# Kernel tuning notes

Measured on AMD Instinct MI355X. Metric: run time of the kernel, lower is better.

## Reference

```python
import jax, jax.numpy as jnp
import numpy as np

B, T, C = 2, 2048, 1024
H, GAMMA = 16, 8
D = C // H
SCALE = 1.0 / np.sqrt(D).astype(np.float32)


def setup_inputs() -> dict:
    key = jax.random.key(0)
    ks = jax.random.split(key, 6)
    w = 0.02
    return {
        'x': jax.random.normal(ks[0], (B, T, C), dtype=jnp.float32),
        'Wq': jax.random.normal(ks[1], (C, 2 * C), dtype=jnp.float32) * w,
        'Wk': jax.random.normal(ks[2], (C, 2 * C), dtype=jnp.float32) * w,
        'Wv': jax.random.normal(ks[3], (C, C), dtype=jnp.float32) * w,
        'Wo': jax.random.normal(ks[4], (C, C), dtype=jnp.float32) * w,
        'theta_offset': jax.random.normal(ks[5], (H,), dtype=jnp.float32) * 0.1,
    }


def _heads(t):
    # (B, T, C) -> (B, H, T, D)
    return t.reshape(B, T, H, D).transpose(0, 2, 1, 3)


def reference(x, Wq, Wk, Wv, Wo, theta_offset):
    q_raw = x @ Wq                      # (B, T, 2C)
    k_raw = x @ Wk                      # (B, T, 2C)
    v = _heads(x @ Wv)                  # (B, H, T, D)

    q_amp, q_phase = jnp.split(q_raw, 2, axis=-1)
    k_amp, k_phase = jnp.split(k_raw, 2, axis=-1)
    q_amp = jax.nn.softplus(_heads(q_amp))
    q_phase = _heads(q_phase)
    k_amp = jax.nn.softplus(_heads(k_amp))
    k_phase = _heads(k_phase)

    q_real = q_amp * jnp.cos(q_phase)
    q_imag = q_amp * jnp.sin(q_phase)
    k_real = k_amp * jnp.cos(k_phase)
    k_imag = k_amp * jnp.sin(k_phase)

    scores = (jnp.einsum('bhtd,bhsd->bhts', q_real, k_real)
              + jnp.einsum('bhtd,bhsd->bhts', q_imag, k_imag)) * SCALE

    # theta gating (active since T > GAMMA)
    cycle_ids = jnp.arange(T, dtype=jnp.float32) / GAMMA
    cycle_dist = cycle_ids[None, :] - cycle_ids[:, None]        # (T, T)
    theta_gate = jnp.cos(theta_offset[:, None, None] * cycle_dist)  # (H, T, T)
    scores = scores * theta_gate[None]

    causal = jnp.tril(jnp.ones((T, T), dtype=bool))
    scores = jnp.where(causal[None, None], scores, -jnp.inf)
    attn = jax.nn.softmax(scores, axis=-1)

    out = jnp.einsum('bhts,bhsd->bhtd', attn, v)
    out = out.transpose(0, 2, 1, 3).reshape(B, T, C)
    return out @ Wo
```

## Files before the change

### kernel.cpp

```cpp
#include <hip/hip_runtime.h>
#include <hip/hip_bf16.h>
#include <math.h>

#define Bc 2
#define Tc 2048
#define Cc 1024
#define Hc 16
#define Dc 64

typedef __attribute__((ext_vector_type(8))) short short8;
typedef __attribute__((ext_vector_type(4))) float f32x4;

#define L2E 1.44269504088896f
#define SM_M 20.0f

__device__ __forceinline__ short f2bf(float x) {
    unsigned u = __float_as_uint(x);
    u += 0x7fff + ((u >> 16) & 1);
    return (short)(u >> 16);
}
__device__ __forceinline__ unsigned pack2bf_fast(float a, float b) {
    unsigned ua = __float_as_uint(a) + 0x8000u;
    unsigned ub = __float_as_uint(b) + 0x8000u;
    return __builtin_amdgcn_perm(ub, ua, 0x07060302);
}
__device__ __forceinline__ float softplus_fast(float a) {
    return fmaxf(a, 0.f) + __logf(1.f + __expf(-fabsf(a)));
}

template <int EPI>
__global__ __launch_bounds__(256) void gemm_bt_mfma(
    const short* __restrict__ A, const short* __restrict__ Bt,
    float* __restrict__ Cf, short* __restrict__ Cb, short* __restrict__ Cb2,
    int M, int N, int K)
{
    __shared__ __attribute__((aligned(16))) short As[128 * 32];
    __shared__ __attribute__((aligned(16))) short Bs[128 * 32];

    const int tid = threadIdx.x;
    const int wave = tid >> 6, lane = tid & 63;
    const int quad = lane >> 4, c = lane & 15;
    const int wm = wave >> 1, wn = wave & 1;
    const int m0 = blockIdx.y * 128, n0 = blockIdx.x * 128;

    const int srow = lane >> 2;
    const int scol = (lane & 3) * 8;
    const short* Ag = A  + (size_t)(m0 + wave * 32 + srow) * K + scol;
    const short* Bg = Bt + (size_t)(n0 + wave * 32 + srow) * K + scol;
    short* AsW = As + (wave * 32) * 32;
    short* BsW = Bs + (wave * 32) * 32;

    f32x4 acc[4][4];
#pragma unroll
    for (int i = 0; i < 4; ++i)
#pragma unroll
        for (int j = 0; j < 4; ++j)
            acc[i][j] = (f32x4){0.f, 0.f, 0.f, 0.f};

    for (int k0 = 0; k0 < K; k0 += 32) {
        __syncthreads();
#pragma unroll
        for (int i = 0; i < 2; ++i) {
            __builtin_amdgcn_global_load_lds(
                (const __attribute__((address_space(1))) void*)(Ag + k0 + (size_t)i * 16 * K),
                (__attribute__((address_space(3))) void*)(AsW + i * 16 * 32), 16, 0, 0);
            __builtin_amdgcn_global_load_lds(
                (const __attribute__((address_space(1))) void*)(Bg + k0 + (size_t)i * 16 * K),
                (__attribute__((address_space(3))) void*)(BsW + i * 16 * 32), 16, 0, 0);
        }
        __syncthreads();

        short8 af[4], bf[4];
#pragma unroll
        for (int mt = 0; mt < 4; ++mt)
            af[mt] = *(const short8*)&As[(wm * 64 + mt * 16 + c) * 32 + quad * 8];
#pragma unroll
        for (int nt = 0; nt < 4; ++nt)
            bf[nt] = *(const short8*)&Bs[(wn * 64 + nt * 16 + c) * 32 + quad * 8];
#pragma unroll
        for (int mt = 0; mt < 4; ++mt)
#pragma unroll
            for (int nt = 0; nt < 4; ++nt)
                acc[mt][nt] = __builtin_amdgcn_mfma_f32_16x16x32_bf16(
                    af[mt], bf[nt], acc[mt][nt], 0, 0, 0);
    }

    if (EPI == 2) {
        const int g = n0 >> 7;
        const int isK = g >> 4;
        const int h = g & 15;
        const float scl = isK ? 1.f : 0.125f;
        short* dst = isK ? Cb2 : Cb;
#pragma unroll
        for (int mt = 0; mt < 4; ++mt) {
#pragma unroll
            for (int reg = 0; reg < 4; ++reg) {
                int m = m0 + wm * 64 + mt * 16 + quad * 4 + reg;
                int bb = m >> 11, tt = m & (Tc - 1);
                size_t base = (((size_t)bb * Hc + h) * Tc + tt) * 128;
#pragma unroll
                for (int nt = 0; nt < 2; ++nt) {
                    float amp = acc[mt][nt][reg];
                    float ph  = acc[mt][nt + 2][reg];
                    int d = wn * 32 + nt * 16 + c;
                    float sp = softplus_fast(amp) * scl;
                    float sn, cs;
                    __sincosf(ph, &sn, &cs);
                    dst[base + d]      = f2bf(sp * cs);
                    dst[base + d + 64] = f2bf(sp * sn);
                }
            }
        }
    } else {
#pragma unroll
        for (int mt = 0; mt < 4; ++mt) {
#pragma unroll
            for (int reg = 0; reg < 4; ++reg) {
                size_t row = m0 + wm * 64 + mt * 16 + quad * 4 + reg;
#pragma unroll
                for (int nt = 0; nt < 4; ++nt) {
                    size_t col = n0 + wn * 64 + nt * 16 + c;
                    if (EPI == 1) Cb[row * N + col] = f2bf(acc[mt][nt][reg]);
                    else          Cf[row * N + col] = acc[mt][nt][reg];
                }
            }
        }
    }
}

__global__ __launch_bounds__(256) void gemm_v2t(
    const short* __restrict__ A, const short* __restrict__ Bt,
    short* __restrict__ v2t)
{
    __shared__ __attribute__((aligned(16))) short As[128 * 32];
    __shared__ __attribute__((aligned(16))) short Bs[128 * 32];
    __shared__ __attribute__((aligned(16))) short tile[128 * 136];

    const int K = Cc;
    const int tid = threadIdx.x;
    const int wave = tid >> 6, lane = tid & 63;
    const int quad = lane >> 4, c = lane & 15;
    const int wm = wave >> 1, wn = wave & 1;
    const int m0 = blockIdx.y * 128, n0 = blockIdx.x * 128;

    const int srow = lane >> 2;
    const int scol = (lane & 3) * 8;
    const short* Ag = A  + (size_t)(m0 + wave * 32 + srow) * K + scol;
    const short* Bg = Bt + (size_t)(n0 + wave * 32 + srow) * K + scol;
    short* AsW = As + (wave * 32) * 32;
    short* BsW = Bs + (wave * 32) * 32;

    f32x4 acc[4][4];
#pragma unroll
    for (int i = 0; i < 4; ++i)
#pragma unroll
        for (int j = 0; j < 4; ++j)
            acc[i][j] = (f32x4){0.f, 0.f, 0.f, 0.f};

    for (int k0 = 0; k0 < K; k0 += 32) {
        __syncthreads();
#pragma unroll
        for (int i = 0; i < 2; ++i) {
            __builtin_amdgcn_global_load_lds(
                (const __attribute__((address_space(1))) void*)(Ag + k0 + (size_t)i * 16 * K),
                (__attribute__((address_space(3))) void*)(AsW + i * 16 * 32), 16, 0, 0);
            __builtin_amdgcn_global_load_lds(
                (const __attribute__((address_space(1))) void*)(Bg + k0 + (size_t)i * 16 * K),
                (__attribute__((address_space(3))) void*)(BsW + i * 16 * 32), 16, 0, 0);
        }
        __syncthreads();

        short8 af[4], bf[4];
#pragma unroll
        for (int mt = 0; mt < 4; ++mt)
            af[mt] = *(const short8*)&As[(wm * 64 + mt * 16 + c) * 32 + quad * 8];
#pragma unroll
        for (int nt = 0; nt < 4; ++nt)
            bf[nt] = *(const short8*)&Bs[(wn * 64 + nt * 16 + c) * 32 + quad * 8];
#pragma unroll
        for (int mt = 0; mt < 4; ++mt)
#pragma unroll
            for (int nt = 0; nt < 4; ++nt)
                acc[mt][nt] = __builtin_amdgcn_mfma_f32_16x16x32_bf16(
                    af[mt], bf[nt], acc[mt][nt], 0, 0, 0);
    }

#pragma unroll
    for (int mt = 0; mt < 4; ++mt)
#pragma unroll
        for (int reg = 0; reg < 4; ++reg) {
            int tl = wm * 64 + mt * 16 + quad * 4 + reg;
#pragma unroll
            for (int nt = 0; nt < 4; ++nt)
                tile[(wn * 64 + nt * 16 + c) * 136 + tl] = f2bf(acc[mt][nt][reg]);
        }
    __syncthreads();

    const int b = m0 >> 11, tl0 = m0 & (Tc - 1);
#pragma unroll
    for (int i = 0; i < 8; ++i) {
        int n = i * 16 + (tid >> 4);
        int t8 = (tid & 15) * 8;
        int ng = n0 + n, h = ng >> 6, d = ng & 63;
        *(short8*)&v2t[(((size_t)b * Hc + h) * Dc + d) * Tc + tl0 + t8] =
            *(const short8*)&tile[n * 136 + t8];
    }
}

__global__ __launch_bounds__(256) void xconv(const float* __restrict__ x,
                                             short* __restrict__ xb)
{
    int idx = blockIdx.x * 256 + threadIdx.x;
    float4 v = *(const float4*)&x[(size_t)idx * 4];
    short4 o = {f2bf(v.x), f2bf(v.y), f2bf(v.z), f2bf(v.w)};
    *(short4*)&xb[(size_t)idx * 4] = o;
}

__global__ __launch_bounds__(256) void wtrans_qk(const float* __restrict__ Wq,
                                                 const float* __restrict__ Wk,
                                                 short* __restrict__ Bt)
{
    __shared__ short tile[64][80];
    const int n0 = blockIdx.x * 64, k0 = blockIdx.y * 64;
    const int half = blockIdx.z;
    const float* W = half ? Wk : Wq;
    const int tid = threadIdx.x;
#pragma unroll
    for (int i = 0; i < 4; ++i) {
        int e = i * 256 + tid;
        int k = e >> 4, n4 = (e & 15) * 4;
        float4 v = *(const float4*)&W[(size_t)(k0 + k) * 2048 + n0 + n4];
        tile[k][n4]     = f2bf(v.x);
        tile[k][n4 + 1] = f2bf(v.y);
        tile[k][n4 + 2] = f2bf(v.z);
        tile[k][n4 + 3] = f2bf(v.w);
    }
    __syncthreads();
#pragma unroll
    for (int i = 0; i < 16; ++i) {
        int e = i * 256 + tid;
        int n = e >> 6, k = e & 63;
        int ng = n0 + n;
        int sub = ng >> 10, hh = (ng >> 6) & 15, dd = ng & 63;
        int r = (half * 16 + hh) * 128 + (dd >> 5) * 64 + sub * 32 + (dd & 31);
        Bt[(size_t)r * Cc + k0 + k] = tile[k][n];
    }
}

__global__ __launch_bounds__(256) void wtrans2(const float* __restrict__ Wv,
                                               const float* __restrict__ Wo,
                                               short* __restrict__ WtBase)
{
    __shared__ short tile[64][80];
    const int n0 = blockIdx.x * 64, k0 = blockIdx.y * 64;
    const float* W = blockIdx.z ? Wo : Wv;
    short* Wt = WtBase + (size_t)blockIdx.z * Cc * Cc;
    const int tid = threadIdx.x;
#pragma unroll
    for (int i = 0; i < 4; ++i) {
        int e = i * 256 + tid;
        int k = e >> 4, n4 = (e & 15) * 4;
        float4 v = *(const float4*)&W[(size_t)(k0 + k) * Cc + n0 + n4];
        tile[k][n4]     = f2bf(v.x);
        tile[k][n4 + 1] = f2bf(v.y);
        tile[k][n4 + 2] = f2bf(v.z);
        tile[k][n4 + 3] = f2bf(v.w);
    }
    __syncthreads();
#pragma unroll
    for (int i = 0; i < 16; ++i) {
        int e = i * 256 + tid;
        int n = e >> 6, k = e & 63;
        Wt[(size_t)(n0 + n) * Cc + k0 + k] = tile[k][n];
    }
}

__global__ __launch_bounds__(512, 4) void moire_attn6(
    const short* __restrict__ q2, const short* __restrict__ k2,
    const short* __restrict__ v2t, const float* __restrict__ theta,
    short* __restrict__ att)
{
    __shared__ __attribute__((aligned(16))) short Ks[2][64 * 128];
    __shared__ __attribute__((aligned(16))) short Vt[2][64 * 64];
    __shared__ __attribute__((aligned(16))) short Ps[8][16 * 64];

    const int tid = threadIdx.x;
    const int wave = tid >> 6, lane = tid & 63;
    const int quad = lane >> 4, c = lane & 15;
    const int tx = wave >> 2, wq = wave & 3;
    const int p = blockIdx.x, h = blockIdx.y, b = blockIdx.z;
    const int qx = tx ? (31 - p) : p;
    const int q0 = qx * 64;
    const float th = theta[h];

    const short* k2b = k2 + (size_t)(b * Hc + h) * Tc * 128;
    const short* v2b = v2t + (size_t)(b * Hc + h) * Dc * Tc;

    short8 qf[4];
    const short* qp = q2 + ((size_t)(b * Hc + h) * Tc + q0 + wq * 16 + c) * 128;
#pragma unroll
    for (int i = 0; i < 4; ++i)
        qf[i] = *(const short8*)(qp + i * 32 + quad * 8);

    const int t_l = wq * 16 + c;
    float x0 = th * 0.125f * (float)(q0 + t_l);
    float cb = __cosf(x0), sb = -__sinf(x0);
    float cOff[4][4], sOff[4][4];
#pragma unroll
    for (int mt = 0; mt < 4; ++mt)
#pragma unroll
        for (int reg = 0; reg < 4; ++reg) {
            float a = th * 0.125f * (float)(mt * 16 + quad * 4 + reg);
            cOff[mt][reg] = __cosf(a) * L2E;
            sOff[mt][reg] = __sinf(a) * L2E;
        }
    const float cD = __cosf(8.f * th), sD = __sinf(8.f * th);

    f32x4 oacc[4];
    float lsum = 0.f;
#pragma unroll
    for (int nt = 0; nt < 4; ++nt)
        oacc[nt] = (f32x4){0.f, 0.f, 0.f, 0.f};

    auto stageK = [&](int jts) {
        short* KsB = &Ks[jts & 1][0];
        const int s0 = jts * 64;
#pragma unroll
        for (int i = 0; i < 2; ++i) {
            int ch = i * 512 + tid;
            int row = ch >> 4, j = ch & 15;
            const short* src = k2b + (size_t)(s0 + row) * 128 + ((j ^ (row & 15)) << 3);
            __builtin_amdgcn_global_load_lds(
                (const __attribute__((address_space(1))) void*)src,
                (__attribute__((address_space(3))) void*)(KsB + (i * 512 + wave * 64) * 8),
                16, 0, 0);
        }
    };
    auto stageV = [&](int jts) {
        short* VtB = &Vt[jts & 1][0];
        const int s0 = jts * 64;
        int row = tid >> 3, j = tid & 7;
        const short* src = v2b + (size_t)row * Tc + s0 + ((j ^ (row & 7)) << 3);
        __builtin_amdgcn_global_load_lds(
            (const __attribute__((address_space(1))) void*)src,
            (__attribute__((address_space(3))) void*)(VtB + (wave * 64) * 8),
            16, 0, 0);
    };

    auto do_pv = [&](int jprev) {
        const short* VtB = &Vt[jprev & 1][0];
        short8 pf[2];
#pragma unroll
        for (int kk = 0; kk < 2; ++kk)
            pf[kk] = *(const short8*)&Ps[wave][c * 64 +
                         (((kk * 4 + quad) ^ (c & 7)) << 3)];
#pragma unroll
        for (int nt = 0; nt < 4; ++nt)
#pragma unroll
            for (int kk = 0; kk < 2; ++kk) {
                short8 vf = *(const short8*)&VtB[(nt * 16 + c) * 64 +
                             (((kk * 4 + quad) ^ (c & 7)) << 3)];
                oacc[nt] = __builtin_amdgcn_mfma_f32_16x16x32_bf16(
                    pf[kk], vf, oacc[nt], 0, 0, 0);
            }
    };

    auto do_s = [&](int jt) {
        const short* KsB = &Ks[jt & 1][0];
        const bool diag = (jt == qx);

        f32x4 s_acc[4];
#pragma unroll
        for (int mt = 0; mt < 4; ++mt) {
            f32x4 a = {0.f, 0.f, 0.f, 0.f};
#pragma unroll
            for (int kk = 0; kk < 4; ++kk) {
                short8 kf = *(const short8*)&KsB[(mt * 16 + c) * 128 +
                                                 (((kk * 4 + quad) ^ c) << 3)];
                a = __builtin_amdgcn_mfma_f32_16x16x32_bf16(kf, qf[kk], a, 0, 0, 0);
            }
            s_acc[mt] = a;
        }

#pragma unroll
        for (int mt = 0; mt < 4; ++mt) {
            float pv[4];
#pragma unroll
            for (int reg = 0; reg < 4; ++reg) {
                float g2 = cb * cOff[mt][reg] - sb * sOff[mt][reg];
                float arg = fmaf(s_acc[mt][reg], g2, -SM_M * L2E);
                if (diag && (mt * 16 + quad * 4 + reg) > t_l) arg = -1e30f;
                pv[reg] = exp2f(arg);
            }
            lsum += (pv[0] + pv[1]) + (pv[2] + pv[3]);
            uint2 pk = {pack2bf_fast(pv[0], pv[1]), pack2bf_fast(pv[2], pv[3])};
            int slot = ((mt * 2 + (quad >> 1)) ^ (c & 7));
            *(uint2*)&Ps[wave][c * 64 + slot * 8 + (quad & 1) * 4] = pk;
        }

        float ncb = cb * cD - sb * sD;
        sb = sb * cD + cb * sD;
        cb = ncb;
    };

    stageK(0);
    const int jtEnd = 31 - p;
    for (int jt = 0; jt <= jtEnd; ++jt) {
        __syncthreads();
        if (jt < jtEnd) stageK(jt + 1);
        stageV(jt);

        const bool doS  = (jt <= qx);
        const bool doPV = (jt >= 1) & (jt <= qx + 1);
        if (doS & doPV) {
            do_pv(jt - 1);
            do_s(jt);
        } else if (doS) {
            do_s(jt);
        } else if (doPV) {
            do_pv(jt - 1);
        }
    }

    __syncthreads();
    if (qx == jtEnd) do_pv(jtEnd);

    float l = lsum;
    l += __shfl_xor(l, 16);
    l += __shfl_xor(l, 32);
    float il = 1.f / l;
    float ilr[4];
#pragma unroll
    for (int reg = 0; reg < 4; ++reg)
        ilr[reg] = __shfl(il, quad * 4 + reg);
#pragma unroll
    for (int reg = 0; reg < 4; ++reg) {
        int t_g = q0 + wq * 16 + quad * 4 + reg;
#pragma unroll
        for (int nt = 0; nt < 4; ++nt)
            att[(size_t)(b * Tc + t_g) * Cc + h * Dc + nt * 16 + c] =
                f2bf(oacc[nt][reg] * ilr[reg]);
    }
}

extern "C" void kernel_launch(void* const* d_in, const int* in_sizes, int n_in,
                              void* d_out, int out_size, void* d_ws, size_t ws_size,
                              hipStream_t stream)
{
    const float* x     = (const float*)d_in[0];
    const float* Wq    = (const float*)d_in[1];
    const float* Wk    = (const float*)d_in[2];
    const float* Wv    = (const float*)d_in[3];
    const float* Wo    = (const float*)d_in[4];
    const float* theta = (const float*)d_in[5];
    float* out = (float*)d_out;

    const int M = Bc * Tc;
    char* ws = (char*)d_ws;
    const size_t MB = 1 << 20;
    short* xb   = (short*)(ws);
    short* Bqk  = (short*)(ws + 8 * MB);
    short* Wvt  = (short*)(ws + 16 * MB);
    short* Wot  = (short*)(ws + 18 * MB);
    short* v2t  = (short*)(ws + 28 * MB);
    short* attb = (short*)(ws + 36 * MB);
    short* q2   = (short*)(ws + 44 * MB);
    short* k2   = (short*)d_out;

    xconv<<<(size_t)M * Cc / 1024, 256, 0, stream>>>(x, xb);
    wtrans_qk<<<dim3(2048 / 64, Cc / 64, 2), 256, 0, stream>>>(Wq, Wk, Bqk);
    wtrans2<<<dim3(Cc / 64, Cc / 64, 2), 256, 0, stream>>>(Wv, Wo, Wvt);

    gemm_bt_mfma<2><<<dim3(4096 / 128, M / 128), 256, 0, stream>>>(
        xb, Bqk, nullptr, q2, k2, M, 4096, Cc);
    gemm_v2t<<<dim3(Cc / 128, M / 128), 256, 0, stream>>>(xb, Wvt, v2t);

    moire_attn6<<<dim3(16, Hc, Bc), 512, 0, stream>>>(q2, k2, v2t, theta, attb);

    gemm_bt_mfma<0><<<dim3(Cc / 128, M / 128), 256, 0, stream>>>(
        attb, Wot, out, nullptr, nullptr, M, Cc, Cc);
}
```

Baseline: 262.2 us.

## Replace QK projection GEMM with 256x256 pipelined direct-to-LDS MFMA kernel

The fused Q/K projection GEMM with its softplus/sincos epilogue moves from a 128x128 tile, 256-thread kernel to a 256x256 tile, 512-thread kernel. The new kernel double-buffers K=64 slices in LDS using global_load_lds with an XOR swizzle, and interleaves loads with MFMA quadrants under explicit barriers, vmcnt waits and setprio. The weight transpose row permutation changes so that amplitude and phase columns land in the new tile layout. The goal is to hide global latency and raise operand reuse in the largest GEMM. The cost is heavy LDS use (128KB per block) and a fragile hand-scheduled barrier and waitcnt pipeline.

```diff
diff --git a/kernel.cpp b/kernel.cpp
--- a/kernel.cpp
+++ b/kernel.cpp
@@ -28,10 +28,164 @@
     return fmaxf(a, 0.f) + __logf(1.f + __expf(-fabsf(a)));
 }
 
+#define RDA(BUF, MH) do {                                                      \
+    const short* Ah_ = &Al[BUF][MH][0];                                        \
+    _Pragma("unroll") for (int mt_ = 0; mt_ < 4; ++mt_) {                      \
+        af[mt_][0] = *(const short8*)&Ah_[(wm*64 + mt_*16 + c)*64 + rsw0];     \
+        af[mt_][1] = *(const short8*)&Ah_[(wm*64 + mt_*16 + c)*64 + rsw1];     \
+    } } while (0)
+
+#define RDB(BUF, NH) do {                                                      \
+    const short* Bh_ = &Bl[BUF][NH][0];                                        \
+    _Pragma("unroll") for (int nf_ = 0; nf_ < 2; ++nf_) {                      \
+        bfr[NH][nf_][0] = *(const short8*)&Bh_[(wn*32 + nf_*16 + c)*64 + rsw0];\
+        bfr[NH][nf_][1] = *(const short8*)&Bh_[(wn*32 + nf_*16 + c)*64 + rsw1];\
+    } } while (0)
+
+#define MMQ(MH, NH) do {                                                       \
+    _Pragma("unroll") for (int mt_ = 0; mt_ < 4; ++mt_)                        \
+    _Pragma("unroll") for (int nf_ = 0; nf_ < 2; ++nf_) {                      \
+        acc[MH][NH][mt_][nf_] = __builtin_amdgcn_mfma_f32_16x16x32_bf16(       \
+            af[mt_][0], bfr[NH][nf_][0], acc[MH][NH][mt_][nf_], 0, 0, 0);      \
+        acc[MH][NH][mt_][nf_] = __builtin_amdgcn_mfma_f32_16x16x32_bf16(       \
+            af[mt_][1], bfr[NH][nf_][1], acc[MH][NH][mt_][nf_], 0, 0, 0);      \
+    } } while (0)
+
+#define BARw asm volatile("s_barrier" ::: "memory")
+#define VMW6 asm volatile("s_waitcnt vmcnt(6)" ::: "memory")
+#define VMW0 asm volatile("s_waitcnt vmcnt(0)" ::: "memory")
+#define PRIO1 __builtin_amdgcn_s_setprio(1)
+#define PRIO0 __builtin_amdgcn_s_setprio(0)
+
+__global__ __launch_bounds__(512, 2) void gemm256_qk(
+    const short* __restrict__ A, const short* __restrict__ Bt,
+    short* __restrict__ q2, short* __restrict__ k2)
+{
+    __shared__ __attribute__((aligned(16))) short Al[2][2][128 * 64];
+    __shared__ __attribute__((aligned(16))) short Bl[2][2][128 * 64];
+
+    const int tid = threadIdx.x;
+    const int wave = tid >> 6, lane = tid & 63;
+    const int quad = lane >> 4, c = lane & 15;
+    const int wm = wave >> 2, wn = wave & 3;
+    const int m0 = blockIdx.y * 256, n0 = blockIdx.x * 256;
+
+    const int rsw0 = ((quad * 16) ^ ((c & 7) << 4)) >> 1;
+    const int rsw1 = ((64 + quad * 16) ^ ((c & 7) << 4)) >> 1;
+
+    f32x4 acc[2][2][4][2];
+#pragma unroll
+    for (int a0 = 0; a0 < 2; ++a0)
+#pragma unroll
+        for (int a1 = 0; a1 < 2; ++a1)
+#pragma unroll
+            for (int a2 = 0; a2 < 4; ++a2)
+#pragma unroll
+                for (int a3 = 0; a3 < 2; ++a3)
+                    acc[a0][a1][a2][a3] = (f32x4){0.f, 0.f, 0.f, 0.f};
+
+    short8 af[4][2];
+    short8 bfr[2][2][2];
+
+    auto stA = [&](int kt, int hh) {
+        short* dstb = &Al[kt & 1][hh][0];
+#pragma unroll
+        for (int j = 0; j < 2; ++j) {
+            int ch = j * 512 + tid;
+            int row = ch >> 3;
+            int os = ((((ch & 7) << 4) ^ ((row & 7) << 4)) >> 1);
+            const short* src = A + (size_t)(m0 + hh * 128 + row) * 1024 + kt * 64 + os;
+            __builtin_amdgcn_global_load_lds(
+                (const __attribute__((address_space(1))) void*)src,
+                (__attribute__((address_space(3))) void*)(dstb + (j * 512 + wave * 64) * 8),
+                16, 0, 0);
+        }
+    };
+    auto stB = [&](int kt, int hh) {
+        short* dstb = &Bl[kt & 1][hh][0];
+#pragma unroll
+        for (int j = 0; j < 2; ++j) {
+            int ch = j * 512 + tid;
+            int row = ch >> 3;
+            int os = ((((ch & 7) << 4) ^ ((row & 7) << 4)) >> 1);
+            const short* src = Bt + (size_t)(n0 + hh * 128 + row) * 1024 + kt * 64 + os;
+            __builtin_amdgcn_global_load_lds(
+                (const __attribute__((address_space(1))) void*)src,
+                (__attribute__((address_space(3))) void*)(dstb + (j * 512 + wave * 64) * 8),
+                16, 0, 0);
+        }
+    };
+
+    stB(0, 0); stA(0, 0); stB(0, 1); stA(0, 1); stB(1, 0); stA(1, 0); stB(1, 1);
+    VMW6;
+    BARw;
+
+    for (int i = 0; i < 8; ++i) {
+        const int e = 2 * i;
+        const bool more = (i < 7);
+        RDA(0, 0); RDB(0, 0);
+        stA(e + 1, 1);
+        BARw; PRIO1; MMQ(0, 0); PRIO0; BARw;
+        RDB(0, 1);
+        if (more) stB(e + 2, 0);
+        BARw; PRIO1; MMQ(0, 1); PRIO0; BARw;
+        RDA(0, 1);
+        if (more) stA(e + 2, 0);
+        BARw; PRIO1; MMQ(1, 0); PRIO0; BARw;
+        if (more) stB(e + 2, 1);
+        BARw; PRIO1; MMQ(1, 1); PRIO0;
+        if (more) { VMW6; } else { VMW0; }
+        BARw;
+        RDA(1, 0); RDB(1, 0);
+        if (more) stA(e + 2, 1);
+        BARw; PRIO1; MMQ(0, 0); PRIO0; BARw;
+        RDB(1, 1);
+        if (more) stB(e + 3, 0);
+        BARw; PRIO1; MMQ(0, 1); PRIO0; BARw;
+        RDA(1, 1);
+        if (more) stA(e + 3, 0);
+        BARw; PRIO1; MMQ(1, 0); PRIO0; BARw;
+        if (more) stB(e + 3, 1);
+        BARw; PRIO1; MMQ(1, 1); PRIO0;
+        if (more) { VMW6; } else { VMW0; }
+        BARw;
+    }
+
+    const int bx = blockIdx.x;
+    const int d = wn * 16 + c;
+#pragma unroll
+    for (int mh = 0; mh < 2; ++mh) {
+#pragma unroll
+        for (int nh = 0; nh < 2; ++nh) {
+            const int g = 2 * bx + nh;
+            const int isK = g >> 4;
+            const int hh = g & 15;
+            const float scl = isK ? 1.f : 0.125f;
+            short* dst = isK ? k2 : q2;
+#pragma unroll
+            for (int mt = 0; mt < 4; ++mt) {
+#pragma unroll
+                for (int reg = 0; reg < 4; ++reg) {
+                    int m = m0 + mh * 128 + wm * 64 + mt * 16 + quad * 4 + reg;
+                    int bb = m >> 11, tt = m & (Tc - 1);
+                    size_t base = (((size_t)bb * Hc + hh) * Tc + tt) * 128;
+                    float amp = acc[mh][nh][mt][0][reg];
+                    float ph  = acc[mh][nh][mt][1][reg];
+                    float sp = softplus_fast(amp) * scl;
+                    float sn, cs;
+                    __sincosf(ph, &sn, &cs);
+                    dst[base + d]      = f2bf(sp * cs);
+                    dst[base + d + 64] = f2bf(sp * sn);
+                }
+            }
+        }
+    }
+}
+
 template <int EPI>
 __global__ __launch_bounds__(256) void gemm_bt_mfma(
     const short* __restrict__ A, const short* __restrict__ Bt,
-    float* __restrict__ Cf, short* __restrict__ Cb, short* __restrict__ Cb2,
+    float* __restrict__ Cf, short* __restrict__ Cb,
     int M, int N, int K)
 {
     __shared__ __attribute__((aligned(16))) short As[128 * 32];
@@ -85,44 +239,16 @@
                     af[mt], bf[nt], acc[mt][nt], 0, 0, 0);
     }
 
-    if (EPI == 2) {
-        const int g = n0 >> 7;
-        const int isK = g >> 4;
-        const int h = g & 15;
-        const float scl = isK ? 1.f : 0.125f;
-        short* dst = isK ? Cb2 : Cb;
-#pragma unroll
-        for (int mt = 0; mt < 4; ++mt) {
-#pragma unroll
-            for (int reg = 0; reg < 4; ++reg) {
-                int m = m0 + wm * 64 + mt * 16 + quad * 4 + reg;
-                int bb = m >> 11, tt = m & (Tc - 1);
-                size_t base = (((size_t)bb * Hc + h) * Tc + tt) * 128;
-#pragma unroll
-                for (int nt = 0; nt < 2; ++nt) {
-                    float amp = acc[mt][nt][reg];
-                    float ph  = acc[mt][nt + 2][reg];
-                    int d = wn * 32 + nt * 16 + c;
-                    float sp = softplus_fast(amp) * scl;
-                    float sn, cs;
-                    __sincosf(ph, &sn, &cs);
-                    dst[base + d]      = f2bf(sp * cs);
-                    dst[base + d + 64] = f2bf(sp * sn);
-                }
-            }
-        }
-    } else {
-#pragma unroll
-        for (int mt = 0; mt < 4; ++mt) {
-#pragma unroll
-            for (int reg = 0; reg < 4; ++reg) {
-                size_t row = m0 + wm * 64 + mt * 16 + quad * 4 + reg;
-#pragma unroll
-                for (int nt = 0; nt < 4; ++nt) {
-                    size_t col = n0 + wn * 64 + nt * 16 + c;
-                    if (EPI == 1) Cb[row * N + col] = f2bf(acc[mt][nt][reg]);
-                    else          Cf[row * N + col] = acc[mt][nt][reg];
-                }
+#pragma unroll
+    for (int mt = 0; mt < 4; ++mt) {
+#pragma unroll
+        for (int reg = 0; reg < 4; ++reg) {
+            size_t row = m0 + wm * 64 + mt * 16 + quad * 4 + reg;
+#pragma unroll
+            for (int nt = 0; nt < 4; ++nt) {
+                size_t col = n0 + wn * 64 + nt * 16 + c;
+                if (EPI == 1) Cb[row * N + col] = f2bf(acc[mt][nt][reg]);
+                else          Cf[row * N + col] = acc[mt][nt][reg];
             }
         }
     }
@@ -242,7 +368,7 @@
         int n = e >> 6, k = e & 63;
         int ng = n0 + n;
         int sub = ng >> 10, hh = (ng >> 6) & 15, dd = ng & 63;
-        int r = (half * 16 + hh) * 128 + (dd >> 5) * 64 + sub * 32 + (dd & 31);
+        int r = (half * 16 + hh) * 128 + (dd >> 4) * 32 + sub * 16 + (dd & 15);
         Bt[(size_t)r * Cc + k0 + k] = tile[k][n];
     }
 }
@@ -471,12 +597,11 @@
     wtrans_qk<<<dim3(2048 / 64, Cc / 64, 2), 256, 0, stream>>>(Wq, Wk, Bqk);
     wtrans2<<<dim3(Cc / 64, Cc / 64, 2), 256, 0, stream>>>(Wv, Wo, Wvt);
 
-    gemm_bt_mfma<2><<<dim3(4096 / 128, M / 128), 256, 0, stream>>>(
-        xb, Bqk, nullptr, q2, k2, M, 4096, Cc);
+    gemm256_qk<<<dim3(4096 / 256, M / 256), 512, 0, stream>>>(xb, Bqk, q2, k2);
     gemm_v2t<<<dim3(Cc / 128, M / 128), 256, 0, stream>>>(xb, Wvt, v2t);
 
     moire_attn6<<<dim3(16, Hc, Bc), 512, 0, stream>>>(q2, k2, v2t, theta, attb);
 
     gemm_bt_mfma<0><<<dim3(Cc / 128, M / 128), 256, 0, stream>>>(
-        attb, Wot, out, nullptr, nullptr, M, Cc, Cc);
-}
+        attb, Wot, out, nullptr, M, Cc, Cc);
+}
```

After: 245.9 us. -6.2%, faster.
